# Performance work log

Hardware: AMD Instinct MI355X
Metric: run time of the kernel (lower is better)

The kernel has to match this reference:

```python
import jax, jax.numpy as jnp
import numpy as np

NHEAD = 8
LN_EPS = 1e-5


def _layernorm(x, g, b):
    mu = jnp.mean(x, -1, keepdims=True)
    var = jnp.mean((x - mu) ** 2, -1, keepdims=True)
    return (x - mu) / jnp.sqrt(var + LN_EPS) * g + b


def _sparse_attn(q, k, v, P):
    # Topology: P queries attend to P keys; G queries attend to P keys + self.
    # q,k,v: [B,H,L,dh], keys/values restricted to pcpt block [B,H,P,dh]
    dh = q.shape[-1]
    scale = 1.0 / jnp.sqrt(jnp.asarray(dh, q.dtype))
    kp, vp = k[:, :, :P], v[:, :, :P]
    S = jnp.einsum('bhld,bhpd->bhlp', q, kp) * scale  # [B,H,L,P]
    # pcpt queries: plain softmax over P keys
    out_p = jnp.einsum('bhqp,bhpd->bhqd', jax.nn.softmax(S[:, :, :P], axis=-1), vp)
    # gen queries: P keys + own diagonal key
    qg, kg, vg = q[:, :, P:], k[:, :, P:], v[:, :, P:]
    Sg = S[:, :, P:]                                   # [B,H,G,P]
    dlog = jnp.sum(qg * kg, -1) * scale                # [B,H,G] diagonal logits
    m = jnp.maximum(jnp.max(Sg, -1), dlog)
    eg = jnp.exp(Sg - m[..., None])
    ed = jnp.exp(dlog - m)
    den = jnp.sum(eg, -1) + ed
    out_g = (jnp.einsum('bhgp,bhpd->bhgd', eg, vp) + ed[..., None] * vg) / den[..., None]
    return jnp.concatenate([out_p, out_g], axis=2)     # [B,H,L,dh]


def _forward(pcpt, gen, Wqkv, bqkv, Wo, bo, W1, b1, W2, b2, g1, beta1, g2, beta2):
    P = pcpt.shape[1]
    x = jnp.concatenate([pcpt, gen], axis=1)           # [B,L,d]
    B, L, d = x.shape
    dh = d // NHEAD
    for i in range(Wqkv.shape[0]):  # post-norm layers
        qkv = (x @ Wqkv[i] + bqkv[i]).reshape(B, L, 3, NHEAD, dh)
        q = jnp.transpose(qkv[:, :, 0], (0, 2, 1, 3))
        k = jnp.transpose(qkv[:, :, 1], (0, 2, 1, 3))
        v = jnp.transpose(qkv[:, :, 2], (0, 2, 1, 3))
        a = _sparse_attn(q, k, v, P)
        a = jnp.transpose(a, (0, 2, 1, 3)).reshape(B, L, d)
        a = a @ Wo[i] + bo[i]
        x = _layernorm(x + a, g1[i], beta1[i])
        h = jax.nn.relu(x @ W1[i] + b1[i]) @ W2[i] + b2[i]
        x = _layernorm(x + h, g2[i], beta2[i])
    return x


def setup_inputs() -> dict:
    key = jax.random.key(0)
    ks = jax.random.split(key, 16)
    B, P, G, d, ff, Lyr = 4, 1024, 1024, 512, 2048, 4
    s = 0.02
    f32 = jnp.float32
    return {
        'pcpt_total_embs': jax.random.normal(ks[0], (B, P, d), f32),
        'gen_total_embs': jax.random.normal(ks[1], (B, G, d), f32),
        'src_key_padding_mask': jnp.zeros((B, P + G), bool),
        'Wqkv': jax.random.normal(ks[2], (Lyr, d, 3 * d), f32) * s,
        'bqkv': jnp.zeros((Lyr, 3 * d), f32),
        'Wo': jax.random.normal(ks[3], (Lyr, d, d), f32) * s,
        'bo': jnp.zeros((Lyr, d), f32),
        'W1': jax.random.normal(ks[4], (Lyr, d, ff), f32) * s,
        'b1': jnp.zeros((Lyr, ff), f32),
        'W2': jax.random.normal(ks[5], (Lyr, ff, d), f32) * s,
        'b2': jnp.zeros((Lyr, d), f32),
        'g1': jnp.ones((Lyr, d), f32),
        'beta1': jnp.zeros((Lyr, d), f32),
        'g2': jnp.ones((Lyr, d), f32),
        'beta2': jnp.zeros((Lyr, d), f32),
    }


def reference(pcpt_total_embs, gen_total_embs, src_key_padding_mask, Wqkv, bqkv, Wo, bo, W1, b1, W2, b2, g1, beta1, g2, beta2):
    P = pcpt_total_embs.shape[1]
    x = _forward(pcpt_total_embs, gen_total_embs, Wqkv, bqkv, Wo, bo, W1, b1, W2, b2, g1, beta1, g2, beta2)
    return x[:, :P], x[:, P:]
```

## Files before the change

kernel.cpp:

```cpp
#include <hip/hip_runtime.h>
#include <hip/hip_bf16.h>

#define B_ 4
#define P_ 1024
#define G_ 1024
#define L_ 2048
#define D_ 512
#define FF_ 2048
#define H_ 8
#define DH_ 64
#define LAYERS_ 4
#define LN_EPS_ 1e-5f

typedef __attribute__((ext_vector_type(8))) short bf16x8;
typedef __attribute__((ext_vector_type(4))) float f32x4;

__device__ __forceinline__ ushort f2b(float f) {
  unsigned u = __float_as_uint(f);
  unsigned r = (u + 0x7fffu + ((u >> 16) & 1u)) >> 16;
  return (ushort)r;
}
__device__ __forceinline__ float b2f(ushort u) {
  return __uint_as_float(((unsigned)u) << 16);
}

__device__ __forceinline__ void gld16(const ushort* g, ushort* l) {
  __builtin_amdgcn_global_load_lds(
      (const __attribute__((address_space(1))) void*)g,
      (__attribute__((address_space(3))) void*)l, 16, 0, 0);
}

__global__ __launch_bounds__(256) void concat_kernel(const float* __restrict__ p,
    const float* __restrict__ g, float* __restrict__ x, ushort* __restrict__ xb)
{
  const int LD4 = L_*D_/4, PD4 = P_*D_/4;
  int i = blockIdx.x*256 + threadIdx.x;
  int b = i / LD4, r = i - b*LD4;
  float4 v;
  if (r < PD4) v = ((const float4*)p)[(size_t)b*PD4 + r];
  else         v = ((const float4*)g)[(size_t)b*PD4 + (r-PD4)];
  ((float4*)x)[i] = v;
  ushort4 h; h.x=f2b(v.x); h.y=f2b(v.y); h.z=f2b(v.z); h.w=f2b(v.w);
  ((ushort4*)xb)[i] = h;
}

__global__ __launch_bounds__(256) void wconv_all(
    const float* __restrict__ Wqkv, const float* __restrict__ Wo,
    const float* __restrict__ W1,   const float* __restrict__ W2,
    ushort* __restrict__ wqkv_b, ushort* __restrict__ wo_b,
    ushort* __restrict__ w1_b,   ushort* __restrict__ w2_b)
{
  __shared__ float tile[32][33];
  int tid = blockIdx.x, l = blockIdx.y;
  const float* src; ushort* dst; int K, N, nx, tloc;
  if (tid < 768)       { src=Wqkv; dst=wqkv_b; K=512;  N=1536; nx=48; tloc=tid; }
  else if (tid < 1024) { src=Wo;   dst=wo_b;   K=512;  N=512;  nx=16; tloc=tid-768; }
  else if (tid < 2048) { src=W1;   dst=w1_b;   K=512;  N=2048; nx=64; tloc=tid-1024; }
  else                 { src=W2;   dst=w2_b;   K=2048; N=512;  nx=16; tloc=tid-2048; }
  int n0 = (tloc % nx)*32, k0 = (tloc / nx)*32;
  src += (size_t)l*K*N; dst += (size_t)l*K*N;
  int tx = threadIdx.x & 31, ty = threadIdx.x >> 5;
  #pragma unroll
  for (int u=0;u<4;++u) tile[ty+8*u][tx] = src[(size_t)(k0+ty+8*u)*N + n0+tx];
  __syncthreads();
  #pragma unroll
  for (int u=0;u<4;++u) dst[(size_t)(n0+ty+8*u)*K + k0+tx] = f2b(tile[tx][ty+8*u]);
}

template<int BN_, int RELU, int RES, int OUTBF, int SPLITK>
__global__ __launch_bounds__(256) void mgemm(
    const ushort* __restrict__ A, const ushort* __restrict__ Bt,
    const float* __restrict__ bias, const float* __restrict__ res,
    void* __restrict__ Cout, float* __restrict__ Cout2, int M, int N, int K)
{
  constexpr int MI = (BN_ == 128) ? 4 : 2;
  constexpr int BL = BN_ / 32;
  __shared__ ushort As[2*128*64];
  __shared__ ushort Bs[2*BN_*64];
  int t = threadIdx.x;
  int lane = t & 63, w = t >> 6;
  int wm = (BN_ == 128) ? (w >> 1) * 64 : w * 32;
  int wn = (BN_ == 128) ? (w & 1) * 64 : 0;
  int m0 = blockIdx.x * 128, n0 = blockIdx.y * BN_;
  const int KS = K / SPLITK;
  int kz = (SPLITK > 1) ? blockIdx.z : 0;

  f32x4 acc[MI][4] = {};

  int rbase = t >> 3;
  int cch   = (t & 7) ^ ((t >> 3) & 7);
  const ushort* Ag = A  + (size_t)(m0 + rbase)*K + kz*KS + cch*8;
  const ushort* Bg = Bt + (size_t)(n0 + rbase)*K + kz*KS + cch*8;
  ushort* Asl0 = As + t*8;
  ushort* Asl1 = As + 128*64 + t*8;
  ushort* Bsl0 = Bs + t*8;
  ushort* Bsl1 = Bs + BN_*64 + t*8;
  const size_t rowK32 = (size_t)32 * K;

  int fr = lane & 15, fq = lane >> 4;
  int swr[2];
  swr[0] = ((0*4 + fq) ^ (fr & 7)) * 8;
  swr[1] = ((1*4 + fq) ^ (fr & 7)) * 8;

  #pragma unroll
  for (int L = 0; L < 4; ++L)  gld16(Ag + L*rowK32, Asl0 + L*2048);
  #pragma unroll
  for (int L = 0; L < BL; ++L) gld16(Bg + L*rowK32, Bsl0 + L*2048);

  const int NT = KS >> 6;
  for (int tt = 0; tt < NT; ++tt) {
    asm volatile("s_waitcnt vmcnt(0)" ::: "memory");
    __builtin_amdgcn_s_barrier();
    __builtin_amdgcn_sched_barrier(0);
    if (tt + 1 < NT) {
      const ushort* Agn = Ag + (size_t)(tt+1)*64;
      const ushort* Bgn = Bg + (size_t)(tt+1)*64;
      ushort* Ad = (tt & 1) ? Asl0 : Asl1;
      ushort* Bd = (tt & 1) ? Bsl0 : Bsl1;
      #pragma unroll
      for (int L = 0; L < 4; ++L)  gld16(Agn + L*rowK32, Ad + L*2048);
      #pragma unroll
      for (int L = 0; L < BL; ++L) gld16(Bgn + L*rowK32, Bd + L*2048);
    }
    const ushort* Ard = ((tt & 1) ? As + 128*64 : As) + (wm + fr)*64;
    const ushort* Brd = ((tt & 1) ? Bs + BN_*64 : Bs) + (wn + fr)*64;
    #pragma unroll
    for (int s = 0; s < 2; ++s) {
      int sw = swr[s];
      bf16x8 af[MI], bfr[4];
      #pragma unroll
      for (int i=0;i<MI;++i) af[i]  = *(const bf16x8*)(Ard + i*16*64 + sw);
      #pragma unroll
      for (int j=0;j<4;++j)  bfr[j] = *(const bf16x8*)(Brd + j*16*64 + sw);
      #pragma unroll
      for (int i=0;i<MI;++i)
        #pragma unroll
        for (int j=0;j<4;++j)
          acc[i][j] = __builtin_amdgcn_mfma_f32_16x16x32_bf16(af[i], bfr[j], acc[i][j], 0, 0, 0);
    }
  }

  int ncol = lane & 15;
  int rquad = (lane >> 4) * 4;
  if (SPLITK > 1 && kz > 0) {
    #pragma unroll
    for (int j=0;j<4;++j) {
      int n = n0 + wn + j*16 + ncol;
      #pragma unroll
      for (int i=0;i<MI;++i) {
        int mbase = m0 + wm + i*16 + rquad;
        #pragma unroll
        for (int r=0;r<4;++r)
          Cout2[(size_t)(mbase+r)*N + n] = acc[i][j][r];
      }
    }
  } else {
    #pragma unroll
    for (int j=0;j<4;++j) {
      int n = n0 + wn + j*16 + ncol;
      float bv = bias[n];
      #pragma unroll
      for (int i=0;i<MI;++i) {
        int mbase = m0 + wm + i*16 + rquad;
        #pragma unroll
        for (int r=0;r<4;++r) {
          int m = mbase + r;
          float c = acc[i][j][r] + bv;
          if (RES) c += res[(size_t)m*N + n];
          if (RELU) c = fmaxf(c, 0.f);
          if (OUTBF) ((ushort*)Cout)[(size_t)m*N + n] = f2b(c);
          else       ((float*)Cout)[(size_t)m*N + n] = c;
        }
      }
    }
  }
}

__global__ __launch_bounds__(256) void mgemm_qkv(
    const ushort* __restrict__ A,
    const ushort* __restrict__ Bt,
    const float* __restrict__ bias,
    ushort* __restrict__ qb,
    ushort* __restrict__ kb,
    ushort* __restrict__ vtb)
{
  const int K = D_;
  __shared__ ushort SMEM[4*128*64];
  ushort* As = SMEM;
  ushort* Bs = SMEM + 2*128*64;
  int t = threadIdx.x;
  int lane = t & 63, w = t >> 6;
  int wm = (w >> 1) * 64, wn = (w & 1) * 64;
  int m0 = blockIdx.x * 128, n0 = blockIdx.y * 128;

  f32x4 acc[4][4] = {};

  int rbase = t >> 3;
  int cch   = (t & 7) ^ ((t >> 3) & 7);
  const ushort* Ag = A  + (size_t)(m0 + rbase)*K + cch*8;
  const ushort* Bg = Bt + (size_t)(n0 + rbase)*K + cch*8;
  ushort* Asl0 = As + t*8;
  ushort* Asl1 = As + 128*64 + t*8;
  ushort* Bsl0 = Bs + t*8;
  ushort* Bsl1 = Bs + 128*64 + t*8;
  const size_t rowK32 = (size_t)32 * K;

  int fr = lane & 15, fq = lane >> 4;
  int swr[2];
  swr[0] = ((0*4 + fq) ^ (fr & 7)) * 8;
  swr[1] = ((1*4 + fq) ^ (fr & 7)) * 8;

  #pragma unroll
  for (int L = 0; L < 4; ++L) gld16(Ag + L*rowK32, Asl0 + L*2048);
  #pragma unroll
  for (int L = 0; L < 4; ++L) gld16(Bg + L*rowK32, Bsl0 + L*2048);

  const int NT = K >> 6;
  for (int tt = 0; tt < NT; ++tt) {
    asm volatile("s_waitcnt vmcnt(0)" ::: "memory");
    __builtin_amdgcn_s_barrier();
    __builtin_amdgcn_sched_barrier(0);
    if (tt + 1 < NT) {
      const ushort* Agn = Ag + (size_t)(tt+1)*64;
      const ushort* Bgn = Bg + (size_t)(tt+1)*64;
      ushort* Ad = (tt & 1) ? Asl0 : Asl1;
      ushort* Bd = (tt & 1) ? Bsl0 : Bsl1;
      #pragma unroll
      for (int L = 0; L < 4; ++L) gld16(Agn + L*rowK32, Ad + L*2048);
      #pragma unroll
      for (int L = 0; L < 4; ++L) gld16(Bgn + L*rowK32, Bd + L*2048);
    }
    const ushort* Ard = ((tt & 1) ? As + 128*64 : As) + (wm + fr)*64;
    const ushort* Brd = ((tt & 1) ? Bs + 128*64 : Bs) + (wn + fr)*64;
    #pragma unroll
    for (int s = 0; s < 2; ++s) {
      int sw = swr[s];
      bf16x8 af[4], bfr[4];
      #pragma unroll
      for (int i=0;i<4;++i) af[i]  = *(const bf16x8*)(Ard + i*16*64 + sw);
      #pragma unroll
      for (int j=0;j<4;++j) bfr[j] = *(const bf16x8*)(Brd + j*16*64 + sw);
      #pragma unroll
      for (int i=0;i<4;++i)
        #pragma unroll
        for (int j=0;j<4;++j)
          acc[i][j] = __builtin_amdgcn_mfma_f32_16x16x32_bf16(af[i], bfr[j], acc[i][j], 0, 0, 0);
    }
  }

  int ncol = lane & 15;
  int rquad = (lane >> 4) * 4;

  if (n0 < 1024) {
    #pragma unroll
    for (int j=0;j<4;++j) {
      int n = n0 + wn + j*16 + ncol;
      float bv = bias[n];
      int part = n >> 9;
      int wi = n & 511;
      int h = wi >> 6, d = wi & 63;
      #pragma unroll
      for (int i=0;i<4;++i) {
        int mbase = m0 + wm + i*16 + rquad;
        #pragma unroll
        for (int r=0;r<4;++r) {
          int m = mbase + r;
          int b = m >> 11, l = m & 2047;
          int bh = b*H_ + h;
          float cv = acc[i][j][r] + bv;
          if (part == 0) cv *= 0.125f;
          ushort c = f2b(cv);
          if (part == 0) qb[((size_t)bh*L_ + l)*DH_ + d] = c;
          else           kb[((size_t)bh*L_ + l)*DH_ + d] = c;
        }
      }
    }
  } else {
    __syncthreads();
    ushort* T = SMEM;
    #pragma unroll
    for (int j=0;j<4;++j) {
      int nrel = wn + j*16 + ncol;
      float bv = bias[n0 + nrel];
      #pragma unroll
      for (int i=0;i<4;++i) {
        #pragma unroll
        for (int r=0;r<4;++r) {
          int mrel = wm + i*16 + rquad + r;
          T[nrel*136 + mrel] = f2b(acc[i][j][r] + bv);
        }
      }
    }
    __syncthreads();
    int b = m0 >> 11, l0r = m0 & 2047;
    int wi0 = n0 & 511;
    #pragma unroll
    for (int u = 0; u < 8; ++u) {
      int idx = u*256 + t;
      int row = idx >> 4, mc = idx & 15;
      uint4 val = *(const uint4*)(T + row*136 + mc*8);
      int wi = wi0 + row;
      int h = wi >> 6, d = wi & 63;
      int bh = b*H_ + h;
      *(uint4*)(vtb + ((size_t)bh*DH_ + d)*L_ + l0r + mc*8) = val;
    }
  }
}

__global__ __launch_bounds__(256) void attn_mfma(
    const ushort* __restrict__ qb, const ushort* __restrict__ kb,
    const ushort* __restrict__ vtb, ushort* __restrict__ outa)
{
  __shared__ ushort Ks[2][64*64];
  __shared__ ushort Vts[2][64*64];
  __shared__ ushort Ps[8*16*72];

  int t = threadIdx.x;
  int lane = t & 63, w = t >> 6;
  int qt = blockIdx.x & 15;
  int h  = (blockIdx.x >> 4) & 7;
  int b  = blockIdx.x >> 7;
  int l0 = qt * 128;
  bool isgen = (l0 >= P_);
  int bh = b*H_ + h;

  const ushort* qg  = qb  + ((size_t)bh*L_ + l0)*DH_;
  const ushort* kgb = kb  + (size_t)bh*L_*DH_;
  const ushort* vtg = vtb + (size_t)bh*DH_*L_;

  int sr  = t >> 3;
  int scg = (t & 7) * 8;
  int scs = ((t & 7) ^ (sr & 7)) * 8;

  int fr = lane & 15, fq = lane >> 4;
  int swz0 = ((0*4 + fq) ^ (fr & 7)) * 8;
  int swz1 = ((1*4 + fq) ^ (fr & 7)) * 8;

  bf16x8 qf[2][2];
  #pragma unroll
  for (int i=0;i<2;++i) {
    qf[i][0] = *(const bf16x8*)(qg + (size_t)(w*32 + i*16 + fr)*DH_ + fq*8);
    qf[i][1] = *(const bf16x8*)(qg + (size_t)(w*32 + i*16 + fr)*DH_ + 32 + fq*8);
  }

  float den[2][4] = {};
  f32x4 o[2][4] = {};
  ushort* Pw0 = Ps + (w*2 + 0)*16*72;
  ushort* Pw1 = Ps + (w*2 + 1)*16*72;

  {
    uint4 a0 = *(const uint4*)(kgb + (size_t)sr*DH_ + scg);
    uint4 a1 = *(const uint4*)(kgb + (size_t)(sr+32)*DH_ + scg);
    uint4 a2 = *(const uint4*)(vtg + (size_t)sr*L_ + scg);
    uint4 a3 = *(const uint4*)(vtg + (size_t)(sr+32)*L_ + scg);
    *(uint4*)(&Ks[0][sr*64 + scs])       = a0;
    *(uint4*)(&Ks[0][(sr+32)*64 + scs])  = a1;
    *(uint4*)(&Vts[0][sr*64 + scs])      = a2;
    *(uint4*)(&Vts[0][(sr+32)*64 + scs]) = a3;
  }
  uint4 pk0 = *(const uint4*)(kgb + (size_t)(64+sr)*DH_ + scg);
  uint4 pk1 = *(const uint4*)(kgb + (size_t)(64+sr+32)*DH_ + scg);
  uint4 pv0 = *(const uint4*)(vtg + (size_t)sr*L_ + 64 + scg);
  uint4 pv1 = *(const uint4*)(vtg + (size_t)(sr+32)*L_ + 64 + scg);
  __syncthreads();

  for (int kt = 0; kt < 16; ++kt) {
    const ushort* Kc = &Ks[kt & 1][0];
    const ushort* Vc = &Vts[kt & 1][0];
    if (kt < 15) {
      ushort* Kn = &Ks[(kt+1) & 1][0];
      ushort* Vn = &Vts[(kt+1) & 1][0];
      *(uint4*)(Kn + sr*64 + scs)      = pk0;
      *(uint4*)(Kn + (sr+32)*64 + scs) = pk1;
      *(uint4*)(Vn + sr*64 + scs)      = pv0;
      *(uint4*)(Vn + (sr+32)*64 + scs) = pv1;
    }
    if (kt < 14) {
      int p2 = (kt + 2) * 64;
      pk0 = *(const uint4*)(kgb + (size_t)(p2+sr)*DH_ + scg);
      pk1 = *(const uint4*)(kgb + (size_t)(p2+sr+32)*DH_ + scg);
      pv0 = *(const uint4*)(vtg + (size_t)sr*L_ + p2 + scg);
      pv1 = *(const uint4*)(vtg + (size_t)(sr+32)*L_ + p2 + scg);
    }

    f32x4 sc4[2][4] = {};
    __builtin_amdgcn_s_setprio(1);
    #pragma unroll
    for (int s=0;s<2;++s) {
      int sw = s ? swz1 : swz0;
      #pragma unroll
      for (int j=0;j<4;++j) {
        bf16x8 kf = *(const bf16x8*)(Kc + (j*16 + fr)*64 + sw);
        sc4[0][j] = __builtin_amdgcn_mfma_f32_16x16x32_bf16(qf[0][s], kf, sc4[0][j], 0, 0, 0);
        sc4[1][j] = __builtin_amdgcn_mfma_f32_16x16x32_bf16(qf[1][s], kf, sc4[1][j], 0, 0, 0);
      }
    }
    __builtin_amdgcn_s_setprio(0);

    #pragma unroll
    for (int i=0;i<2;++i) {
      ushort* Pw = i ? Pw1 : Pw0;
      #pragma unroll
      for (int r=0;r<4;++r) {
        float e0 = __expf(sc4[i][0][r]);
        float e1 = __expf(sc4[i][1][r]);
        float e2 = __expf(sc4[i][2][r]);
        float e3 = __expf(sc4[i][3][r]);
        den[i][r] += (e0+e1) + (e2+e3);
        Pw[(fq*4+r)*72 +  0 + fr] = (ushort)(__float_as_uint(e0) >> 16);
        Pw[(fq*4+r)*72 + 16 + fr] = (ushort)(__float_as_uint(e1) >> 16);
        Pw[(fq*4+r)*72 + 32 + fr] = (ushort)(__float_as_uint(e2) >> 16);
        Pw[(fq*4+r)*72 + 48 + fr] = (ushort)(__float_as_uint(e3) >> 16);
      }
    }
    asm volatile("s_waitcnt lgkmcnt(0)" ::: "memory");

    __builtin_amdgcn_s_setprio(1);
    #pragma unroll
    for (int s=0;s<2;++s) {
      int sw = s ? swz1 : swz0;
      bf16x8 pf0 = *(const bf16x8*)(Pw0 + fr*72 + s*32 + fq*8);
      bf16x8 pf1 = *(const bf16x8*)(Pw1 + fr*72 + s*32 + fq*8);
      #pragma unroll
      for (int j=0;j<4;++j) {
        bf16x8 vf = *(const bf16x8*)(Vc + (j*16 + fr)*64 + sw);
        o[0][j] = __builtin_amdgcn_mfma_f32_16x16x32_bf16(pf0, vf, o[0][j], 0, 0, 0);
        o[1][j] = __builtin_amdgcn_mfma_f32_16x16x32_bf16(pf1, vf, o[1][j], 0, 0, 0);
      }
    }
    __builtin_amdgcn_s_setprio(0);
    __syncthreads();
  }

  #pragma unroll
  for (int i=0;i<2;++i)
    #pragma unroll
    for (int r=0;r<4;++r) {
      float d = den[i][r];
      d += __shfl_xor(d, 1, 16);
      d += __shfl_xor(d, 2, 16);
      d += __shfl_xor(d, 4, 16);
      d += __shfl_xor(d, 8, 16);
      den[i][r] = d;
    }

  if (isgen) {
    #pragma unroll
    for (int i=0;i<2;++i) {
      int base = l0 + w*32 + i*16;
      f32x4 dsc = {};
      {
        bf16x8 kd0 = *(const bf16x8*)(kgb + (size_t)(base + fr)*DH_ + fq*8);
        dsc = __builtin_amdgcn_mfma_f32_16x16x32_bf16(qf[i][0], kd0, dsc, 0, 0, 0);
        bf16x8 kd1 = *(const bf16x8*)(kgb + (size_t)(base + fr)*DH_ + 32 + fq*8);
        dsc = __builtin_amdgcn_mfma_f32_16x16x32_bf16(qf[i][1], kd1, dsc, 0, 0, 0);
      }
      #pragma unroll
      for (int r=0;r<4;++r) {
        int m = fq*4 + r;
        float dl = __shfl(dsc[r], fq*16 + m);
        float ed = __expf(dl);
        den[i][r] += ed;
        int l = base + m;
        #pragma unroll
        for (int j=0;j<4;++j) {
          float vv = b2f(vtg[(size_t)(j*16 + fr)*L_ + l]);
          o[i][j][r] += ed*vv;
        }
      }
    }
  }

  #pragma unroll
  for (int i=0;i<2;++i)
    #pragma unroll
    for (int r=0;r<4;++r) {
      float inv = 1.f / den[i][r];
      int l = l0 + w*32 + i*16 + fq*4 + r;
      #pragma unroll
      for (int j=0;j<4;++j)
        outa[((size_t)b*L_ + l)*D_ + h*DH_ + j*16 + fr] = f2b(o[i][j][r]*inv);
    }
}

template<int FINAL>
__global__ __launch_bounds__(256) void ln_kernel(const float* __restrict__ y,
    const float* __restrict__ y2,
    const float* __restrict__ gw, const float* __restrict__ bw,
    float* __restrict__ x, ushort* __restrict__ xb, float* __restrict__ outf)
{
  int w = threadIdx.x >> 6, t = threadIdx.x & 63;
  int row = blockIdx.x*4 + w;
  const float4* yr = (const float4*)(y + (size_t)row*D_);
  float4 v0 = yr[t], v1 = yr[t+64];
  if (y2) {
    const float4* y2r = (const float4*)(y2 + (size_t)row*D_);
    float4 a0 = y2r[t], a1 = y2r[t+64];
    v0.x+=a0.x; v0.y+=a0.y; v0.z+=a0.z; v0.w+=a0.w;
    v1.x+=a1.x; v1.y+=a1.y; v1.z+=a1.z; v1.w+=a1.w;
  }
  float s = v0.x+v0.y+v0.z+v0.w + v1.x+v1.y+v1.z+v1.w;
  for (int off=32; off>0; off>>=1) s += __shfl_down(s, off, 64);
  s = __shfl(s, 0, 64);
  float mu = s * (1.f/D_);
  float dx;
  float q = 0.f;
  dx=v0.x-mu; q+=dx*dx; dx=v0.y-mu; q+=dx*dx; dx=v0.z-mu; q+=dx*dx; dx=v0.w-mu; q+=dx*dx;
  dx=v1.x-mu; q+=dx*dx; dx=v1.y-mu; q+=dx*dx; dx=v1.z-mu; q+=dx*dx; dx=v1.w-mu; q+=dx*dx;
  for (int off=32; off>0; off>>=1) q += __shfl_down(q, off, 64);
  q = __shfl(q, 0, 64);
  float rinv = rsqrtf(q*(1.f/D_) + LN_EPS_);
  const float4* g4 = (const float4*)gw;
  const float4* b4 = (const float4*)bw;
  float4 gv0=g4[t], gv1=g4[t+64], bv0=b4[t], bv1=b4[t+64];
  float4 o0, o1;
  o0.x=(v0.x-mu)*rinv*gv0.x+bv0.x; o0.y=(v0.y-mu)*rinv*gv0.y+bv0.y;
  o0.z=(v0.z-mu)*rinv*gv0.z+bv0.z; o0.w=(v0.w-mu)*rinv*gv0.w+bv0.w;
  o1.x=(v1.x-mu)*rinv*gv1.x+bv1.x; o1.y=(v1.y-mu)*rinv*gv1.y+bv1.y;
  o1.z=(v1.z-mu)*rinv*gv1.z+bv1.z; o1.w=(v1.w-mu)*rinv*gv1.w+bv1.w;
  if (FINAL) {
    int b = row >> 11, l = row & 2047;
    int orow = (l < P_) ? (b*P_ + l) : (B_*P_ + b*G_ + (l - P_));
    float4* orp = (float4*)(outf + (size_t)orow*D_);
    orp[t] = o0; orp[t+64] = o1;
  } else {
    float4* xr = (float4*)(x + (size_t)row*D_);
    xr[t]=o0; xr[t+64]=o1;
    ushort4 h0, h1;
    h0.x=f2b(o0.x); h0.y=f2b(o0.y); h0.z=f2b(o0.z); h0.w=f2b(o0.w);
    h1.x=f2b(o1.x); h1.y=f2b(o1.y); h1.z=f2b(o1.z); h1.w=f2b(o1.w);
    ushort4* xbr = (ushort4*)(xb + (size_t)row*D_);
    xbr[t]=h0; xbr[t+64]=h1;
  }
}

extern "C" void kernel_launch(void* const* d_in, const int* in_sizes, int n_in,
                              void* d_out, int out_size, void* d_ws, size_t ws_size,
                              hipStream_t stream) {
  const float* pcpt = (const float*)d_in[0];
  const float* gen  = (const float*)d_in[1];
  const float* Wqkv = (const float*)d_in[3];
  const float* bqkv = (const float*)d_in[4];
  const float* Wo   = (const float*)d_in[5];
  const float* bo   = (const float*)d_in[6];
  const float* W1   = (const float*)d_in[7];
  const float* b1   = (const float*)d_in[8];
  const float* W2   = (const float*)d_in[9];
  const float* b2   = (const float*)d_in[10];
  const float* g1   = (const float*)d_in[11];
  const float* be1  = (const float*)d_in[12];
  const float* g2   = (const float*)d_in[13];
  const float* be2  = (const float*)d_in[14];
  float* out = (float*)d_out;

  const size_t XD  = (size_t)B_*L_*D_;
  const size_t HKV = (size_t)B_*H_*L_*DH_;
  const size_t HFF = (size_t)B_*L_*FF_;

  float*  xbuf = (float*)d_ws;
  ushort* xbf  = (ushort*)(xbuf + XD);
  ushort* region = xbf + XD;
  ushort* qb  = region;
  ushort* kb  = region + HKV;
  ushort* vtb = region + 2*HKV;
  ushort* hbf = region;
  ushort* abf = region + HFF;
  ushort* wb  = abf + XD;
  ushort* wqkv_b = wb;
  ushort* wo_b   = wqkv_b + (size_t)4*3*D_*D_;
  ushort* w1_b   = wo_b   + (size_t)4*D_*D_;
  ushort* w2_b   = w1_b   + (size_t)4*FF_*D_;
  float*  ybuf   = (float*)(w2_b + (size_t)4*D_*FF_);
  float*  y2buf  = ybuf + XD;

  const int M = B_*L_;

  wconv_all<<<dim3(3072, 4), 256, 0, stream>>>(
      Wqkv, Wo, W1, W2, wqkv_b, wo_b, w1_b, w2_b);

  concat_kernel<<<4096, 256, 0, stream>>>(pcpt, gen, xbuf, xbf);

  for (int i = 0; i < LAYERS_; ++i) {
    const ushort* wqkv_i = wqkv_b + (size_t)i*3*D_*D_;
    const ushort* wo_i   = wo_b   + (size_t)i*D_*D_;
    const ushort* w1_i   = w1_b   + (size_t)i*FF_*D_;
    const ushort* w2_i   = w2_b   + (size_t)i*D_*FF_;
    const float* bqkv_i = bqkv + (size_t)i*3*D_;
    const float* bo_i   = bo   + (size_t)i*D_;
    const float* b1_i   = b1   + (size_t)i*FF_;
    const float* b2_i   = b2   + (size_t)i*D_;
    const float* g1_i   = g1   + (size_t)i*D_;
    const float* be1_i  = be1  + (size_t)i*D_;
    const float* g2_i   = g2   + (size_t)i*D_;
    const float* be2_i  = be2  + (size_t)i*D_;

    mgemm_qkv<<<dim3(M/128, 3*D_/128), 256, 0, stream>>>(
        xbf, wqkv_i, bqkv_i, qb, kb, vtb);

    attn_mfma<<<B_*H_*(L_/128), 256, 0, stream>>>(qb, kb, vtb, abf);

    mgemm<64,0,1,0,1><<<dim3(M/128, D_/64), 256, 0, stream>>>(
        abf, wo_i, bo_i, xbuf, ybuf, nullptr, M, D_, D_);

    ln_kernel<0><<<M/4, 256, 0, stream>>>(
        ybuf, nullptr, g1_i, be1_i, xbuf, xbf, nullptr);

    mgemm<128,1,0,1,1><<<dim3(M/128, FF_/128), 256, 0, stream>>>(
        xbf, w1_i, b1_i, nullptr, hbf, nullptr, M, FF_, D_);

    mgemm<64,0,1,0,2><<<dim3(M/128, D_/64, 2), 256, 0, stream>>>(
        hbf, w2_i, b2_i, xbuf, ybuf, y2buf, M, D_, FF_);

    if (i == LAYERS_-1)
      ln_kernel<1><<<M/4, 256, 0, stream>>>(
          ybuf, y2buf, g2_i, be2_i, nullptr, nullptr, out);
    else
      ln_kernel<0><<<M/4, 256, 0, stream>>>(
          ybuf, y2buf, g2_i, be2_i, xbuf, xbf, nullptr);
  }
}
```

Baseline: 715.5 us.

## Stage GEMM tiles through registers with two-deep prefetch instead of direct-to-LDS loads

```diff
diff --git a/kernel.cpp b/kernel.cpp
--- a/kernel.cpp
+++ b/kernel.cpp
@@ -75,8 +75,9 @@
 {
   constexpr int MI = (BN_ == 128) ? 4 : 2;
   constexpr int BL = BN_ / 32;
-  __shared__ ushort As[2*128*64];
-  __shared__ ushort Bs[2*BN_*64];
+  constexpr int ATILE = 128*64, BTILE = BN_*64;
+  __shared__ ushort As[2*ATILE];
+  __shared__ ushort Bs[2*BTILE];
   int t = threadIdx.x;
   int lane = t & 63, w = t >> 6;
   int wm = (BN_ == 128) ? (w >> 1) * 64 : w * 32;
@@ -91,10 +92,6 @@
   int cch   = (t & 7) ^ ((t >> 3) & 7);
   const ushort* Ag = A  + (size_t)(m0 + rbase)*K + kz*KS + cch*8;
   const ushort* Bg = Bt + (size_t)(n0 + rbase)*K + kz*KS + cch*8;
-  ushort* Asl0 = As + t*8;
-  ushort* Asl1 = As + 128*64 + t*8;
-  ushort* Bsl0 = Bs + t*8;
-  ushort* Bsl1 = Bs + BN_*64 + t*8;
   const size_t rowK32 = (size_t)32 * K;
 
   int fr = lane & 15, fq = lane >> 4;
@@ -102,28 +99,44 @@
   swr[0] = ((0*4 + fq) ^ (fr & 7)) * 8;
   swr[1] = ((1*4 + fq) ^ (fr & 7)) * 8;
 
-  #pragma unroll
-  for (int L = 0; L < 4; ++L)  gld16(Ag + L*rowK32, Asl0 + L*2048);
-  #pragma unroll
-  for (int L = 0; L < BL; ++L) gld16(Bg + L*rowK32, Bsl0 + L*2048);
-
+  uint4 rA[4], rB[BL];
   const int NT = KS >> 6;
+
+  #pragma unroll
+  for (int L = 0; L < 4; ++L)  rA[L] = *(const uint4*)(Ag + L*rowK32);
+  #pragma unroll
+  for (int L = 0; L < BL; ++L) rB[L] = *(const uint4*)(Bg + L*rowK32);
+  #pragma unroll
+  for (int L = 0; L < 4; ++L)  *(uint4*)(As + t*8 + L*2048) = rA[L];
+  #pragma unroll
+  for (int L = 0; L < BL; ++L) *(uint4*)(Bs + t*8 + L*2048) = rB[L];
+  if (NT > 1) {
+    #pragma unroll
+    for (int L = 0; L < 4; ++L)  rA[L] = *(const uint4*)(Ag + 64 + L*rowK32);
+    #pragma unroll
+    for (int L = 0; L < BL; ++L) rB[L] = *(const uint4*)(Bg + 64 + L*rowK32);
+  }
+  __syncthreads();
+
   for (int tt = 0; tt < NT; ++tt) {
-    asm volatile("s_waitcnt vmcnt(0)" ::: "memory");
-    __builtin_amdgcn_s_barrier();
-    __builtin_amdgcn_sched_barrier(0);
     if (tt + 1 < NT) {
-      const ushort* Agn = Ag + (size_t)(tt+1)*64;
-      const ushort* Bgn = Bg + (size_t)(tt+1)*64;
-      ushort* Ad = (tt & 1) ? Asl0 : Asl1;
-      ushort* Bd = (tt & 1) ? Bsl0 : Bsl1;
-      #pragma unroll
-      for (int L = 0; L < 4; ++L)  gld16(Agn + L*rowK32, Ad + L*2048);
-      #pragma unroll
-      for (int L = 0; L < BL; ++L) gld16(Bgn + L*rowK32, Bd + L*2048);
-    }
-    const ushort* Ard = ((tt & 1) ? As + 128*64 : As) + (wm + fr)*64;
-    const ushort* Brd = ((tt & 1) ? Bs + BN_*64 : Bs) + (wn + fr)*64;
+      ushort* Ad = As + ((tt+1)&1)*ATILE + t*8;
+      ushort* Bd = Bs + ((tt+1)&1)*BTILE + t*8;
+      #pragma unroll
+      for (int L = 0; L < 4; ++L)  *(uint4*)(Ad + L*2048) = rA[L];
+      #pragma unroll
+      for (int L = 0; L < BL; ++L) *(uint4*)(Bd + L*2048) = rB[L];
+    }
+    if (tt + 2 < NT) {
+      const ushort* Agn = Ag + (size_t)(tt+2)*64;
+      const ushort* Bgn = Bg + (size_t)(tt+2)*64;
+      #pragma unroll
+      for (int L = 0; L < 4; ++L)  rA[L] = *(const uint4*)(Agn + L*rowK32);
+      #pragma unroll
+      for (int L = 0; L < BL; ++L) rB[L] = *(const uint4*)(Bgn + L*rowK32);
+    }
+    const ushort* Ard = As + (tt&1)*ATILE + (wm + fr)*64;
+    const ushort* Brd = Bs + (tt&1)*BTILE + (wn + fr)*64;
     #pragma unroll
     for (int s = 0; s < 2; ++s) {
       int sw = swr[s];
@@ -138,6 +151,8 @@
         for (int j=0;j<4;++j)
           acc[i][j] = __builtin_amdgcn_mfma_f32_16x16x32_bf16(af[i], bfr[j], acc[i][j], 0, 0, 0);
     }
+    asm volatile("s_waitcnt lgkmcnt(0)" ::: "memory");
+    __builtin_amdgcn_s_barrier();
   }
 
   int ncol = lane & 15;
```

Measured after the change: 1.265 ms. 1.77x slower.
